# Kernel optimization log

Measured on AMD Instinct MI355X. Metric: run time of the kernel, lower is better.

## Reference

```python
import jax, jax.numpy as jnp
import numpy as np

B, S, D = 4, 2048, 1024
H = 16
HD = D // H

def setup_inputs() -> dict:
    key = jax.random.key(0)
    ks = jax.random.split(key, 6)
    std = 1.0 / np.sqrt(D)
    x = jax.random.normal(ks[0], (B, S, D), dtype=jnp.float32)
    Wq = jax.random.uniform(ks[1], (D, D), jnp.float32, -std, std)
    Wk = jax.random.uniform(ks[2], (D, D), jnp.float32, -std, std)
    Wv = jax.random.uniform(ks[3], (D, D), jnp.float32, -std, std)
    Wo = jax.random.uniform(ks[4], (D, D), jnp.float32, -std, std)
    bo = jax.random.uniform(ks[5], (D,), jnp.float32, -std, std)
    return {"x": x, "Wq": Wq, "Wk": Wk, "Wv": Wv, "Wo": Wo, "bo": bo}

def reference(x, Wq, Wk, Wv, Wo, bo):
    b, s, _ = x.shape
    # projections; torch Linear computes x @ W^T, here W stored as (d_in, d_out)... we use (D, D) applied as x @ W
    q = (x @ Wq).reshape(b, s, H, HD).transpose(0, 2, 1, 3)  # b h s hd
    k = (x @ Wk).reshape(b, s, H, HD).transpose(0, 2, 1, 3)
    v = (x @ Wv).reshape(b, s, H, HD).transpose(0, 2, 1, 3)
    scores = jnp.einsum('bhqd,bhkd->bhqk', q, k)
    causal = jnp.triu(jnp.ones((s, s), dtype=bool), k=1)
    scores = jnp.where(causal[None, None], -jnp.inf, scores)
    attn = jax.nn.softmax(scores / np.sqrt(HD), axis=-1)  # dropout=0.0 -> identity
    ctx = jnp.einsum('bhqk,bhkd->bhqd', attn, v)
    ctx = ctx.transpose(0, 2, 1, 3).reshape(b, s, D)
    return ctx @ Wo + bo
```

## Files before the change

kernel.cpp:

```cpp
#include <hip/hip_runtime.h>

typedef unsigned short u16;
typedef __bf16 bf16x8 __attribute__((ext_vector_type(8)));
typedef float f32x4 __attribute__((ext_vector_type(4)));

#define Bn 4
#define Sn 2048
#define Dn 1024
#define Hn 16
#define HDn 64

__device__ inline u16 f2bf(float f) {
  unsigned u = __builtin_bit_cast(unsigned, f);
  u += 0x7fffu + ((u >> 16) & 1u);
  return (u16)(u >> 16);
}

__device__ __forceinline__ void gl2lds16(const u16* g, u16* l) {
  __builtin_amdgcn_global_load_lds(
      (const __attribute__((address_space(1))) unsigned int*)g,
      (__attribute__((address_space(3))) unsigned int*)l, 16, 0, 0);
}

__device__ __forceinline__ float fexp2(float x) {
  return __builtin_amdgcn_exp2f(x);
}

__device__ __forceinline__ unsigned pk_bf_trunc(float lo, float hi) {
  return __builtin_amdgcn_perm(__builtin_bit_cast(unsigned, hi),
                               __builtin_bit_cast(unsigned, lo), 0x07060302u);
}

__global__ __launch_bounds__(256) void cvt4(const float* __restrict__ in,
                                            u16* __restrict__ out, int n4) {
  int i = blockIdx.x * 256 + threadIdx.x;
  if (i < n4) {
    float4 v = ((const float4*)in)[i];
    ushort4 o;
    o.x = f2bf(v.x); o.y = f2bf(v.y); o.z = f2bf(v.z); o.w = f2bf(v.w);
    ((ushort4*)out)[i] = o;
  }
}

__global__ __launch_bounds__(256) void tcvt(const float* __restrict__ in,
                                            u16* __restrict__ out, int n) {
  __shared__ u16 tile[32][33];
  int bx = blockIdx.x * 32;
  int by = blockIdx.y * 32;
  int tx = threadIdx.x & 31;
  int ty = threadIdx.x >> 5;
#pragma unroll
  for (int r = 0; r < 32; r += 8)
    tile[ty + r][tx] = f2bf(in[(size_t)(by + ty + r) * n + bx + tx]);
  __syncthreads();
#pragma unroll
  for (int r = 0; r < 32; r += 8)
    out[(size_t)(bx + ty + r) * n + by + tx] = tile[tx][ty + r];
}

__global__ __launch_bounds__(256) void gemm_qkv(const u16* __restrict__ A,
                                                const u16* __restrict__ Bt,
                                                u16* __restrict__ qkb,
                                                u16* __restrict__ vt,
                                                float qscale) {
  __shared__ __attribute__((aligned(16))) u16 As[128][32];
  __shared__ __attribute__((aligned(16))) u16 Bs[128][32];
  const int K = Dn;
  const int t = threadIdx.x;
  const int wave = t >> 6;
  const int lane = t & 63;
  const int lcol = lane & 15;
  const int quad = lane >> 4;
  const int wm = (wave >> 1) * 64;
  const int wn = (wave & 1) * 64;
  const int bm = blockIdx.y * 128;
  const int bn = blockIdx.x * 128;

  const int srow = lane >> 2;
  const int sseg = (lane & 3) * 8;
  const u16* a0p = A + (size_t)(bm + wave * 16 + srow) * K + sseg;
  const u16* a1p = a0p + (size_t)64 * K;
  const u16* b0p = Bt + (size_t)(bn + wave * 16 + srow) * K + sseg;
  const u16* b1p = b0p + (size_t)64 * K;
  u16* asl0 = &As[0][0] + wave * 512 + lane * 8;
  u16* asl1 = asl0 + 2048;
  u16* bsl0 = &Bs[0][0] + wave * 512 + lane * 8;
  u16* bsl1 = bsl0 + 2048;

  f32x4 acc[4][4];
#pragma unroll
  for (int i = 0; i < 4; i++)
#pragma unroll
    for (int j = 0; j < 4; j++) acc[i][j] = (f32x4){0.f, 0.f, 0.f, 0.f};

  for (int k0 = 0; k0 < K; k0 += 32) {
    gl2lds16(a0p + k0, asl0);
    gl2lds16(a1p + k0, asl1);
    gl2lds16(b0p + k0, bsl0);
    gl2lds16(b1p + k0, bsl1);
    __syncthreads();
    bf16x8 af[4], bf[4];
#pragma unroll
    for (int mi = 0; mi < 4; mi++)
      af[mi] = *(const bf16x8*)(&As[wm + mi * 16 + lcol][quad * 8]);
#pragma unroll
    for (int ni = 0; ni < 4; ni++)
      bf[ni] = *(const bf16x8*)(&Bs[wn + ni * 16 + lcol][quad * 8]);
#pragma unroll
    for (int mi = 0; mi < 4; mi++)
#pragma unroll
      for (int ni = 0; ni < 4; ni++)
        acc[mi][ni] = __builtin_amdgcn_mfma_f32_16x16x32_bf16(af[mi], bf[ni], acc[mi][ni], 0, 0, 0);
    __syncthreads();
  }

  if (bn >= 2048) {
    const int b = bm >> 11;
#pragma unroll
    for (int mi = 0; mi < 4; mi++) {
#pragma unroll
      for (int ni = 0; ni < 4; ni++) {
        int row0 = bm + wm + mi * 16 + quad * 4;
        int s = row0 & (Sn - 1);
        int vcol = bn + wn + ni * 16 + lcol - 2048;
        int bh = (b << 4) + (vcol >> 6);
        int hd = vcol & 63;
        unsigned d0 = (unsigned)f2bf(acc[mi][ni][0]) |
                      ((unsigned)f2bf(acc[mi][ni][1]) << 16);
        unsigned d1 = (unsigned)f2bf(acc[mi][ni][2]) |
                      ((unsigned)f2bf(acc[mi][ni][3]) << 16);
        *(uint2*)(vt + ((size_t)bh * HDn + hd) * Sn + s) = (uint2){d0, d1};
      }
    }
  } else {
    const float scale = (bn < 1024) ? qscale : 1.0f;
#pragma unroll
    for (int mi = 0; mi < 4; mi++) {
#pragma unroll
      for (int ni = 0; ni < 4; ni++) {
#pragma unroll
        for (int r = 0; r < 4; r++) {
          int row = bm + wm + mi * 16 + quad * 4 + r;
          int col = bn + wn + ni * 16 + lcol;
          qkb[(size_t)row * 2048 + col] = f2bf(acc[mi][ni][r] * scale);
        }
      }
    }
  }
}

__global__ __launch_bounds__(256) void gemm_out(const u16* __restrict__ A,
                                                const u16* __restrict__ Bt,
                                                float* __restrict__ Cout,
                                                const float* __restrict__ bias) {
  __shared__ __attribute__((aligned(16))) u16 As[128][32];
  __shared__ __attribute__((aligned(16))) u16 Bs[64][32];
  const int K = Dn;
  const int t = threadIdx.x;
  const int wave = t >> 6;
  const int lane = t & 63;
  const int lcol = lane & 15;
  const int quad = lane >> 4;
  const int wm = (wave >> 1) * 64;
  const int wn = (wave & 1) * 32;
  const int bm = blockIdx.y * 128;
  const int bn = blockIdx.x * 64;

  const int srow = lane >> 2;
  const int sseg = (lane & 3) * 8;
  const u16* a0p = A + (size_t)(bm + wave * 16 + srow) * K + sseg;
  const u16* a1p = a0p + (size_t)64 * K;
  const u16* b0p = Bt + (size_t)(bn + wave * 16 + srow) * K + sseg;
  u16* asl0 = &As[0][0] + wave * 512 + lane * 8;
  u16* asl1 = asl0 + 2048;
  u16* bsl0 = &Bs[0][0] + wave * 512 + lane * 8;

  f32x4 acc[4][2];
#pragma unroll
  for (int i = 0; i < 4; i++)
#pragma unroll
    for (int j = 0; j < 2; j++) acc[i][j] = (f32x4){0.f, 0.f, 0.f, 0.f};

  for (int k0 = 0; k0 < K; k0 += 32) {
    gl2lds16(a0p + k0, asl0);
    gl2lds16(a1p + k0, asl1);
    gl2lds16(b0p + k0, bsl0);
    __syncthreads();
    bf16x8 af[4], bf[2];
#pragma unroll
    for (int mi = 0; mi < 4; mi++)
      af[mi] = *(const bf16x8*)(&As[wm + mi * 16 + lcol][quad * 8]);
#pragma unroll
    for (int ni = 0; ni < 2; ni++)
      bf[ni] = *(const bf16x8*)(&Bs[wn + ni * 16 + lcol][quad * 8]);
#pragma unroll
    for (int mi = 0; mi < 4; mi++)
#pragma unroll
      for (int ni = 0; ni < 2; ni++)
        acc[mi][ni] = __builtin_amdgcn_mfma_f32_16x16x32_bf16(af[mi], bf[ni], acc[mi][ni], 0, 0, 0);
    __syncthreads();
  }

#pragma unroll
  for (int mi = 0; mi < 4; mi++) {
#pragma unroll
    for (int ni = 0; ni < 2; ni++) {
#pragma unroll
      for (int r = 0; r < 4; r++) {
        int row = bm + wm + mi * 16 + quad * 4 + r;
        int col = bn + wn + ni * 16 + lcol;
        Cout[(size_t)row * Dn + col] = acc[mi][ni][r] + bias[col];
      }
    }
  }
}

__global__ __launch_bounds__(256, 4) void attn4(const u16* __restrict__ QK,
                                                const u16* __restrict__ Vt,
                                                u16* __restrict__ ctx) {
  __shared__ __attribute__((aligned(16))) u16 Ks2[2][64][32];
  __shared__ __attribute__((aligned(16))) u16 Vts2[2][64][32];
  __shared__ __attribute__((aligned(16))) u16 Pt[4][32][72];

  const int bh = blockIdx.x;
  const int b = bh >> 4, h = bh & 15;
  const int q0 = (15 - blockIdx.y) * 128;
  const int t = threadIdx.x;
  const int w = t >> 6;
  const int lane = t & 63;
  const int lcol = lane & 15;
  const int quad = lane >> 4;
  const int qw = q0 + w * 32;

  const size_t qkbase = ((size_t)b * Sn) * 2048 + h * HDn;
  const size_t obase = ((size_t)b * Sn) * Dn + h * HDn;
  const size_t vbase = ((size_t)bh * HDn) * Sn;

  bf16x8 qf[2][2];
#pragma unroll
  for (int qb = 0; qb < 2; qb++) {
    const u16* qp = QK + qkbase + (size_t)(qw + qb * 16 + lcol) * 2048 + quad * 8;
    qf[qb][0] = *(const bf16x8*)qp;
    qf[qb][1] = *(const bf16x8*)(qp + 32);
  }

  f32x4 o[2][4];
#pragma unroll
  for (int qb = 0; qb < 2; qb++)
#pragma unroll
    for (int nb = 0; nb < 4; nb++) o[qb][nb] = (f32x4){0.f, 0.f, 0.f, 0.f};
  float lsum[2] = {0.f, 0.f};

  const int srow = lane >> 2;
  const int sseg = (lane & 3) * 8;
  const u16* kp0 = QK + qkbase + 1024 + (size_t)(w * 16 + srow) * 2048 + sseg;
  const u16* vp0 = Vt + vbase + (size_t)(w * 16 + srow) * Sn + sseg;
  u16* ksl0 = &Ks2[0][0][0] + w * 512 + lane * 8;
  u16* ksl1 = ksl0 + 2048;
  u16* vsl0 = &Vts2[0][0][0] + w * 512 + lane * 8;
  u16* vsl1 = vsl0 + 2048;

  const int n_kv = q0 + 128;

  for (int j0 = 0; j0 < n_kv; j0 += 64) {
    {
      const u16* kp = kp0 + (size_t)j0 * 2048;
      gl2lds16(kp, ksl0);
      gl2lds16(kp + 32, ksl1);
      const u16* vp = vp0 + j0;
      gl2lds16(vp, vsl0);
      gl2lds16(vp + 32, vsl1);
    }
    __syncthreads();

    if (j0 <= qw + 31) {
      f32x4 s[4][2];
#pragma unroll
      for (int mb = 0; mb < 4; mb++) {
        bf16x8 kf0 = *(const bf16x8*)(&Ks2[0][mb * 16 + lcol][quad * 8]);
        bf16x8 kf1 = *(const bf16x8*)(&Ks2[1][mb * 16 + lcol][quad * 8]);
#pragma unroll
        for (int qb = 0; qb < 2; qb++) {
          f32x4 a = (f32x4){0.f, 0.f, 0.f, 0.f};
          a = __builtin_amdgcn_mfma_f32_16x16x32_bf16(kf0, qf[qb][0], a, 0, 0, 0);
          a = __builtin_amdgcn_mfma_f32_16x16x32_bf16(kf1, qf[qb][1], a, 0, 0, 0);
          s[mb][qb] = a;
        }
      }

      const bool needmask = (j0 + 63 > qw);
#pragma unroll
      for (int qb = 0; qb < 2; qb++) {
        const int qrow = qw + qb * 16 + lcol;
#pragma unroll
        for (int mb = 0; mb < 4; mb++) {
          float p[4];
#pragma unroll
          for (int r = 0; r < 4; r++) p[r] = fexp2(s[mb][qb][r]);
          if (needmask) {
            const int kvb = j0 + mb * 16 + quad * 4;
#pragma unroll
            for (int r = 0; r < 4; r++)
              if (kvb + r > qrow) p[r] = 0.f;
          }
          lsum[qb] += (p[0] + p[1]) + (p[2] + p[3]);
          unsigned d0 = pk_bf_trunc(p[0], p[1]);
          unsigned d1 = pk_bf_trunc(p[2], p[3]);
          *(uint2*)(&Pt[w][qb * 16 + lcol][mb * 16 + quad * 4]) = (uint2){d0, d1};
        }
      }

#pragma unroll
      for (int c = 0; c < 2; c++) {
        bf16x8 pf0 = *(const bf16x8*)(&Pt[w][lcol][c * 32 + quad * 8]);
        bf16x8 pf1 = *(const bf16x8*)(&Pt[w][16 + lcol][c * 32 + quad * 8]);
#pragma unroll
        for (int nb = 0; nb < 4; nb++) {
          bf16x8 vf = *(const bf16x8*)(&Vts2[c][nb * 16 + lcol][quad * 8]);
          o[0][nb] = __builtin_amdgcn_mfma_f32_16x16x32_bf16(vf, pf0, o[0][nb], 0, 0, 0);
          o[1][nb] = __builtin_amdgcn_mfma_f32_16x16x32_bf16(vf, pf1, o[1][nb], 0, 0, 0);
        }
      }
    }
    __syncthreads();
  }

#pragma unroll
  for (int qb = 0; qb < 2; qb++) {
    float l = lsum[qb];
    l += __shfl_xor(l, 16);
    l += __shfl_xor(l, 32);
    float inv = 1.0f / l;
#pragma unroll
    for (int nb = 0; nb < 4; nb++) {
      unsigned d0 = (unsigned)f2bf(o[qb][nb][0] * inv) |
                    ((unsigned)f2bf(o[qb][nb][1] * inv) << 16);
      unsigned d1 = (unsigned)f2bf(o[qb][nb][2] * inv) |
                    ((unsigned)f2bf(o[qb][nb][3] * inv) << 16);
      u16* p = ctx + obase + (size_t)(qw + qb * 16 + lcol) * Dn + nb * 16 + quad * 4;
      *(uint2*)p = (uint2){d0, d1};
    }
  }
}

extern "C" void kernel_launch(void* const* d_in, const int* in_sizes, int n_in,
                              void* d_out, int out_size, void* d_ws, size_t ws_size,
                              hipStream_t stream) {
  const float* x  = (const float*)d_in[0];
  const float* Wq = (const float*)d_in[1];
  const float* Wk = (const float*)d_in[2];
  const float* Wv = (const float*)d_in[3];
  const float* Wo = (const float*)d_in[4];
  const float* bo = (const float*)d_in[5];
  float* out = (float*)d_out;

  const size_t BSD = (size_t)Bn * Sn * Dn;
  const size_t DD = (size_t)Dn * Dn;

  u16* xb    = (u16*)d_ws;
  u16* wqkvt = xb + BSD;
  u16* wot   = wqkvt + 3 * DD;
  u16* qkb   = wot + DD;
  u16* vt    = qkb + 2 * BSD;
  u16* cb    = vt + BSD;

  cvt4<<<(int)(BSD / 4 / 256), 256, 0, stream>>>(x, xb, (int)(BSD / 4));
  dim3 tg(Dn / 32, Dn / 32);
  tcvt<<<tg, 256, 0, stream>>>(Wq, wqkvt, Dn);
  tcvt<<<tg, 256, 0, stream>>>(Wk, wqkvt + DD, Dn);
  tcvt<<<tg, 256, 0, stream>>>(Wv, wqkvt + 2 * DD, Dn);
  tcvt<<<tg, 256, 0, stream>>>(Wo, wot, Dn);

  gemm_qkv<<<dim3(3072 / 128, (Bn * Sn) / 128), 256, 0, stream>>>(
      xb, wqkvt, qkb, vt, 0.125f * 1.44269504f);

  attn4<<<dim3(Bn * Hn, 16), 256, 0, stream>>>(qkb, vt, cb);

  gemm_out<<<dim3(Dn / 64, (Bn * Sn) / 128), 256, 0, stream>>>(cb, wot, out, bo);
}
```

Measured before the change: 263.8 us.

## Pair causal query tiles in attention, deepen GEMM K-step, merge weight conversions

The attention kernel now gives each block two query tiles, one near the start and one near the end of the sequence, so every block does balanced causal work, and it halves the grid to 8 blocks per head. The K/V tile loaded into shared memory is reused by both strips. Both GEMMs now load 64 K-elements per barrier pair instead of 32, halving synchronisations at the cost of doubled LDS. The four weight transpose-converts are merged into one launch with a z-dimension. Risks are higher register pressure in attention (launch bounds lowered to 2) and fewer blocks in flight.

Result: faster. 246.7 us (-6.5%).

```diff
diff --git a/kernel.cpp b/kernel.cpp
--- a/kernel.cpp
+++ b/kernel.cpp
@@ -42,20 +42,26 @@
   }
 }
 
-__global__ __launch_bounds__(256) void tcvt(const float* __restrict__ in,
-                                            u16* __restrict__ out, int n) {
+__global__ __launch_bounds__(256) void tcvt4(const float* __restrict__ w0,
+                                             const float* __restrict__ w1,
+                                             const float* __restrict__ w2,
+                                             const float* __restrict__ w3,
+                                             u16* __restrict__ out) {
   __shared__ u16 tile[32][33];
+  const float* in = (blockIdx.z == 0) ? w0 : (blockIdx.z == 1) ? w1
+                   : (blockIdx.z == 2) ? w2 : w3;
+  u16* dst = out + (size_t)blockIdx.z * Dn * Dn;
   int bx = blockIdx.x * 32;
   int by = blockIdx.y * 32;
   int tx = threadIdx.x & 31;
   int ty = threadIdx.x >> 5;
 #pragma unroll
   for (int r = 0; r < 32; r += 8)
-    tile[ty + r][tx] = f2bf(in[(size_t)(by + ty + r) * n + bx + tx]);
+    tile[ty + r][tx] = f2bf(in[(size_t)(by + ty + r) * Dn + bx + tx]);
   __syncthreads();
 #pragma unroll
   for (int r = 0; r < 32; r += 8)
-    out[(size_t)(bx + ty + r) * n + by + tx] = tile[tx][ty + r];
+    dst[(size_t)(bx + ty + r) * Dn + by + tx] = tile[tx][ty + r];
 }
 
 __global__ __launch_bounds__(256) void gemm_qkv(const u16* __restrict__ A,
@@ -63,8 +69,8 @@
                                                 u16* __restrict__ qkb,
                                                 u16* __restrict__ vt,
                                                 float qscale) {
-  __shared__ __attribute__((aligned(16))) u16 As[128][32];
-  __shared__ __attribute__((aligned(16))) u16 Bs[128][32];
+  __shared__ __attribute__((aligned(16))) u16 As[2][128][32];
+  __shared__ __attribute__((aligned(16))) u16 Bs[2][128][32];
   const int K = Dn;
   const int t = threadIdx.x;
   const int wave = t >> 6;
@@ -82,9 +88,9 @@
   const u16* a1p = a0p + (size_t)64 * K;
   const u16* b0p = Bt + (size_t)(bn + wave * 16 + srow) * K + sseg;
   const u16* b1p = b0p + (size_t)64 * K;
-  u16* asl0 = &As[0][0] + wave * 512 + lane * 8;
+  u16* asl0 = &As[0][0][0] + wave * 512 + lane * 8;
   u16* asl1 = asl0 + 2048;
-  u16* bsl0 = &Bs[0][0] + wave * 512 + lane * 8;
+  u16* bsl0 = &Bs[0][0][0] + wave * 512 + lane * 8;
   u16* bsl1 = bsl0 + 2048;
 
   f32x4 acc[4][4];
@@ -93,24 +99,31 @@
 #pragma unroll
     for (int j = 0; j < 4; j++) acc[i][j] = (f32x4){0.f, 0.f, 0.f, 0.f};
 
-  for (int k0 = 0; k0 < K; k0 += 32) {
+  for (int k0 = 0; k0 < K; k0 += 64) {
     gl2lds16(a0p + k0, asl0);
     gl2lds16(a1p + k0, asl1);
+    gl2lds16(a0p + k0 + 32, asl0 + 4096);
+    gl2lds16(a1p + k0 + 32, asl1 + 4096);
     gl2lds16(b0p + k0, bsl0);
     gl2lds16(b1p + k0, bsl1);
-    __syncthreads();
-    bf16x8 af[4], bf[4];
-#pragma unroll
-    for (int mi = 0; mi < 4; mi++)
-      af[mi] = *(const bf16x8*)(&As[wm + mi * 16 + lcol][quad * 8]);
-#pragma unroll
-    for (int ni = 0; ni < 4; ni++)
-      bf[ni] = *(const bf16x8*)(&Bs[wn + ni * 16 + lcol][quad * 8]);
-#pragma unroll
-    for (int mi = 0; mi < 4; mi++)
+    gl2lds16(b0p + k0 + 32, bsl0 + 4096);
+    gl2lds16(b1p + k0 + 32, bsl1 + 4096);
+    __syncthreads();
+#pragma unroll
+    for (int ks = 0; ks < 2; ks++) {
+      bf16x8 af[4], bf[4];
+#pragma unroll
+      for (int mi = 0; mi < 4; mi++)
+        af[mi] = *(const bf16x8*)(&As[ks][wm + mi * 16 + lcol][quad * 8]);
 #pragma unroll
       for (int ni = 0; ni < 4; ni++)
-        acc[mi][ni] = __builtin_amdgcn_mfma_f32_16x16x32_bf16(af[mi], bf[ni], acc[mi][ni], 0, 0, 0);
+        bf[ni] = *(const bf16x8*)(&Bs[ks][wn + ni * 16 + lcol][quad * 8]);
+#pragma unroll
+      for (int mi = 0; mi < 4; mi++)
+#pragma unroll
+        for (int ni = 0; ni < 4; ni++)
+          acc[mi][ni] = __builtin_amdgcn_mfma_f32_16x16x32_bf16(af[mi], bf[ni], acc[mi][ni], 0, 0, 0);
+    }
     __syncthreads();
   }
 
@@ -153,8 +166,8 @@
                                                 const u16* __restrict__ Bt,
                                                 float* __restrict__ Cout,
                                                 const float* __restrict__ bias) {
-  __shared__ __attribute__((aligned(16))) u16 As[128][32];
-  __shared__ __attribute__((aligned(16))) u16 Bs[64][32];
+  __shared__ __attribute__((aligned(16))) u16 As[2][128][32];
+  __shared__ __attribute__((aligned(16))) u16 Bs[2][64][32];
   const int K = Dn;
   const int t = threadIdx.x;
   const int wave = t >> 6;
@@ -171,9 +184,9 @@
   const u16* a0p = A + (size_t)(bm + wave * 16 + srow) * K + sseg;
   const u16* a1p = a0p + (size_t)64 * K;
   const u16* b0p = Bt + (size_t)(bn + wave * 16 + srow) * K + sseg;
-  u16* asl0 = &As[0][0] + wave * 512 + lane * 8;
+  u16* asl0 = &As[0][0][0] + wave * 512 + lane * 8;
   u16* asl1 = asl0 + 2048;
-  u16* bsl0 = &Bs[0][0] + wave * 512 + lane * 8;
+  u16* bsl0 = &Bs[0][0][0] + wave * 512 + lane * 8;
 
   f32x4 acc[4][2];
 #pragma unroll
@@ -181,23 +194,29 @@
 #pragma unroll
     for (int j = 0; j < 2; j++) acc[i][j] = (f32x4){0.f, 0.f, 0.f, 0.f};
 
-  for (int k0 = 0; k0 < K; k0 += 32) {
+  for (int k0 = 0; k0 < K; k0 += 64) {
     gl2lds16(a0p + k0, asl0);
     gl2lds16(a1p + k0, asl1);
+    gl2lds16(a0p + k0 + 32, asl0 + 4096);
+    gl2lds16(a1p + k0 + 32, asl1 + 4096);
     gl2lds16(b0p + k0, bsl0);
-    __syncthreads();
-    bf16x8 af[4], bf[2];
-#pragma unroll
-    for (int mi = 0; mi < 4; mi++)
-      af[mi] = *(const bf16x8*)(&As[wm + mi * 16 + lcol][quad * 8]);
-#pragma unroll
-    for (int ni = 0; ni < 2; ni++)
-      bf[ni] = *(const bf16x8*)(&Bs[wn + ni * 16 + lcol][quad * 8]);
-#pragma unroll
-    for (int mi = 0; mi < 4; mi++)
+    gl2lds16(b0p + k0 + 32, bsl0 + 2048);
+    __syncthreads();
+#pragma unroll
+    for (int ks = 0; ks < 2; ks++) {
+      bf16x8 af[4], bf[2];
+#pragma unroll
+      for (int mi = 0; mi < 4; mi++)
+        af[mi] = *(const bf16x8*)(&As[ks][wm + mi * 16 + lcol][quad * 8]);
 #pragma unroll
       for (int ni = 0; ni < 2; ni++)
-        acc[mi][ni] = __builtin_amdgcn_mfma_f32_16x16x32_bf16(af[mi], bf[ni], acc[mi][ni], 0, 0, 0);
+        bf[ni] = *(const bf16x8*)(&Bs[ks][wn + ni * 16 + lcol][quad * 8]);
+#pragma unroll
+      for (int mi = 0; mi < 4; mi++)
+#pragma unroll
+        for (int ni = 0; ni < 2; ni++)
+          acc[mi][ni] = __builtin_amdgcn_mfma_f32_16x16x32_bf16(af[mi], bf[ni], acc[mi][ni], 0, 0, 0);
+    }
     __syncthreads();
   }
 
@@ -215,7 +234,7 @@
   }
 }
 
-__global__ __launch_bounds__(256, 4) void attn4(const u16* __restrict__ QK,
+__global__ __launch_bounds__(256, 2) void attn5(const u16* __restrict__ QK,
                                                 const u16* __restrict__ Vt,
                                                 u16* __restrict__ ctx) {
   __shared__ __attribute__((aligned(16))) u16 Ks2[2][64][32];
@@ -224,32 +243,39 @@
 
   const int bh = blockIdx.x;
   const int b = bh >> 4, h = bh & 15;
-  const int q0 = (15 - blockIdx.y) * 128;
+  const int pair = blockIdx.y;
   const int t = threadIdx.x;
   const int w = t >> 6;
   const int lane = t & 63;
   const int lcol = lane & 15;
   const int quad = lane >> 4;
-  const int qw = q0 + w * 32;
+  const int qw0 = pair * 128 + w * 32;
+  const int qw1 = (15 - pair) * 128 + w * 32;
 
   const size_t qkbase = ((size_t)b * Sn) * 2048 + h * HDn;
   const size_t obase = ((size_t)b * Sn) * Dn + h * HDn;
   const size_t vbase = ((size_t)bh * HDn) * Sn;
 
-  bf16x8 qf[2][2];
-#pragma unroll
-  for (int qb = 0; qb < 2; qb++) {
-    const u16* qp = QK + qkbase + (size_t)(qw + qb * 16 + lcol) * 2048 + quad * 8;
-    qf[qb][0] = *(const bf16x8*)qp;
-    qf[qb][1] = *(const bf16x8*)(qp + 32);
-  }
-
-  f32x4 o[2][4];
-#pragma unroll
-  for (int qb = 0; qb < 2; qb++)
-#pragma unroll
-    for (int nb = 0; nb < 4; nb++) o[qb][nb] = (f32x4){0.f, 0.f, 0.f, 0.f};
-  float lsum[2] = {0.f, 0.f};
+  bf16x8 qf[2][2][2];
+#pragma unroll
+  for (int si = 0; si < 2; si++) {
+    const int qws = si ? qw1 : qw0;
+#pragma unroll
+    for (int qb = 0; qb < 2; qb++) {
+      const u16* qp = QK + qkbase + (size_t)(qws + qb * 16 + lcol) * 2048 + quad * 8;
+      qf[si][qb][0] = *(const bf16x8*)qp;
+      qf[si][qb][1] = *(const bf16x8*)(qp + 32);
+    }
+  }
+
+  f32x4 o[2][2][4];
+#pragma unroll
+  for (int si = 0; si < 2; si++)
+#pragma unroll
+    for (int qb = 0; qb < 2; qb++)
+#pragma unroll
+      for (int nb = 0; nb < 4; nb++) o[si][qb][nb] = (f32x4){0.f, 0.f, 0.f, 0.f};
+  float lsum[2][2] = {{0.f, 0.f}, {0.f, 0.f}};
 
   const int srow = lane >> 2;
   const int sseg = (lane & 3) * 8;
@@ -260,7 +286,57 @@
   u16* vsl0 = &Vts2[0][0][0] + w * 512 + lane * 8;
   u16* vsl1 = vsl0 + 2048;
 
-  const int n_kv = q0 + 128;
+  auto do_strip = [&](int si, int qw, int j0) {
+    f32x4 s[4][2];
+#pragma unroll
+    for (int mb = 0; mb < 4; mb++) {
+      bf16x8 kf0 = *(const bf16x8*)(&Ks2[0][mb * 16 + lcol][quad * 8]);
+      bf16x8 kf1 = *(const bf16x8*)(&Ks2[1][mb * 16 + lcol][quad * 8]);
+#pragma unroll
+      for (int qb = 0; qb < 2; qb++) {
+        f32x4 a = (f32x4){0.f, 0.f, 0.f, 0.f};
+        a = __builtin_amdgcn_mfma_f32_16x16x32_bf16(kf0, qf[si][qb][0], a, 0, 0, 0);
+        a = __builtin_amdgcn_mfma_f32_16x16x32_bf16(kf1, qf[si][qb][1], a, 0, 0, 0);
+        s[mb][qb] = a;
+      }
+    }
+
+    const bool needmask = (j0 + 63 > qw);
+#pragma unroll
+    for (int qb = 0; qb < 2; qb++) {
+      const int qrow = qw + qb * 16 + lcol;
+#pragma unroll
+      for (int mb = 0; mb < 4; mb++) {
+        float p[4];
+#pragma unroll
+        for (int r = 0; r < 4; r++) p[r] = fexp2(s[mb][qb][r]);
+        if (needmask) {
+          const int kvb = j0 + mb * 16 + quad * 4;
+#pragma unroll
+          for (int r = 0; r < 4; r++)
+            if (kvb + r > qrow) p[r] = 0.f;
+        }
+        lsum[si][qb] += (p[0] + p[1]) + (p[2] + p[3]);
+        unsigned d0 = pk_bf_trunc(p[0], p[1]);
+        unsigned d1 = pk_bf_trunc(p[2], p[3]);
+        *(uint2*)(&Pt[w][qb * 16 + lcol][mb * 16 + quad * 4]) = (uint2){d0, d1};
+      }
+    }
+
+#pragma unroll
+    for (int c = 0; c < 2; c++) {
+      bf16x8 pf0 = *(const bf16x8*)(&Pt[w][lcol][c * 32 + quad * 8]);
+      bf16x8 pf1 = *(const bf16x8*)(&Pt[w][16 + lcol][c * 32 + quad * 8]);
+#pragma unroll
+      for (int nb = 0; nb < 4; nb++) {
+        bf16x8 vf = *(const bf16x8*)(&Vts2[c][nb * 16 + lcol][quad * 8]);
+        o[si][0][nb] = __builtin_amdgcn_mfma_f32_16x16x32_bf16(vf, pf0, o[si][0][nb], 0, 0, 0);
+        o[si][1][nb] = __builtin_amdgcn_mfma_f32_16x16x32_bf16(vf, pf1, o[si][1][nb], 0, 0, 0);
+      }
+    }
+  };
+
+  const int n_kv = (15 - pair) * 128 + 128;
 
   for (int j0 = 0; j0 < n_kv; j0 += 64) {
     {
@@ -273,72 +349,29 @@
     }
     __syncthreads();
 
-    if (j0 <= qw + 31) {
-      f32x4 s[4][2];
-#pragma unroll
-      for (int mb = 0; mb < 4; mb++) {
-        bf16x8 kf0 = *(const bf16x8*)(&Ks2[0][mb * 16 + lcol][quad * 8]);
-        bf16x8 kf1 = *(const bf16x8*)(&Ks2[1][mb * 16 + lcol][quad * 8]);
-#pragma unroll
-        for (int qb = 0; qb < 2; qb++) {
-          f32x4 a = (f32x4){0.f, 0.f, 0.f, 0.f};
-          a = __builtin_amdgcn_mfma_f32_16x16x32_bf16(kf0, qf[qb][0], a, 0, 0, 0);
-          a = __builtin_amdgcn_mfma_f32_16x16x32_bf16(kf1, qf[qb][1], a, 0, 0, 0);
-          s[mb][qb] = a;
-        }
-      }
-
-      const bool needmask = (j0 + 63 > qw);
-#pragma unroll
-      for (int qb = 0; qb < 2; qb++) {
-        const int qrow = qw + qb * 16 + lcol;
-#pragma unroll
-        for (int mb = 0; mb < 4; mb++) {
-          float p[4];
-#pragma unroll
-          for (int r = 0; r < 4; r++) p[r] = fexp2(s[mb][qb][r]);
-          if (needmask) {
-            const int kvb = j0 + mb * 16 + quad * 4;
-#pragma unroll
-            for (int r = 0; r < 4; r++)
-              if (kvb + r > qrow) p[r] = 0.f;
-          }
-          lsum[qb] += (p[0] + p[1]) + (p[2] + p[3]);
-          unsigned d0 = pk_bf_trunc(p[0], p[1]);
-          unsigned d1 = pk_bf_trunc(p[2], p[3]);
-          *(uint2*)(&Pt[w][qb * 16 + lcol][mb * 16 + quad * 4]) = (uint2){d0, d1};
-        }
-      }
-
-#pragma unroll
-      for (int c = 0; c < 2; c++) {
-        bf16x8 pf0 = *(const bf16x8*)(&Pt[w][lcol][c * 32 + quad * 8]);
-        bf16x8 pf1 = *(const bf16x8*)(&Pt[w][16 + lcol][c * 32 + quad * 8]);
-#pragma unroll
-        for (int nb = 0; nb < 4; nb++) {
-          bf16x8 vf = *(const bf16x8*)(&Vts2[c][nb * 16 + lcol][quad * 8]);
-          o[0][nb] = __builtin_amdgcn_mfma_f32_16x16x32_bf16(vf, pf0, o[0][nb], 0, 0, 0);
-          o[1][nb] = __builtin_amdgcn_mfma_f32_16x16x32_bf16(vf, pf1, o[1][nb], 0, 0, 0);
-        }
-      }
-    }
-    __syncthreads();
-  }
-
-#pragma unroll
-  for (int qb = 0; qb < 2; qb++) {
-    float l = lsum[qb];
-    l += __shfl_xor(l, 16);
-    l += __shfl_xor(l, 32);
-    float inv = 1.0f / l;
-#pragma unroll
-    for (int nb = 0; nb < 4; nb++) {
-      unsigned d0 = (unsigned)f2bf(o[qb][nb][0] * inv) |
-                    ((unsigned)f2bf(o[qb][nb][1] * inv) << 16);
-      unsigned d1 = (unsigned)f2bf(o[qb][nb][2] * inv) |
-                    ((unsigned)f2bf(o[qb][nb][3] * inv) << 16);
-      u16* p = ctx + obase + (size_t)(qw + qb * 16 + lcol) * Dn + nb * 16 + quad * 4;
-      *(uint2*)p = (uint2){d0, d1};
+    if (j0 <= qw1 + 31) do_strip(1, qw1, j0);
+    if (j0 <= qw0 + 31) do_strip(0, qw0, j0);
+    __syncthreads();
+  }
+
+#pragma unroll
+  for (int si = 0; si < 2; si++) {
+    const int qws = si ? qw1 : qw0;
+#pragma unroll
+    for (int qb = 0; qb < 2; qb++) {
+      float l = lsum[si][qb];
+      l += __shfl_xor(l, 16);
+      l += __shfl_xor(l, 32);
+      float inv = 1.0f / l;
+#pragma unroll
+      for (int nb = 0; nb < 4; nb++) {
+        unsigned d0 = (unsigned)f2bf(o[si][qb][nb][0] * inv) |
+                      ((unsigned)f2bf(o[si][qb][nb][1] * inv) << 16);
+        unsigned d1 = (unsigned)f2bf(o[si][qb][nb][2] * inv) |
+                      ((unsigned)f2bf(o[si][qb][nb][3] * inv) << 16);
+        u16* p = ctx + obase + (size_t)(qws + qb * 16 + lcol) * Dn + nb * 16 + quad * 4;
+        *(uint2*)p = (uint2){d0, d1};
+      }
     }
   }
 }
@@ -358,23 +391,18 @@
   const size_t DD = (size_t)Dn * Dn;
 
   u16* xb    = (u16*)d_ws;
-  u16* wqkvt = xb + BSD;
-  u16* wot   = wqkvt + 3 * DD;
-  u16* qkb   = wot + DD;
+  u16* wall  = xb + BSD;
+  u16* qkb   = wall + 4 * DD;
   u16* vt    = qkb + 2 * BSD;
   u16* cb    = vt + BSD;
 
   cvt4<<<(int)(BSD / 4 / 256), 256, 0, stream>>>(x, xb, (int)(BSD / 4));
-  dim3 tg(Dn / 32, Dn / 32);
-  tcvt<<<tg, 256, 0, stream>>>(Wq, wqkvt, Dn);
-  tcvt<<<tg, 256, 0, stream>>>(Wk, wqkvt + DD, Dn);
-  tcvt<<<tg, 256, 0, stream>>>(Wv, wqkvt + 2 * DD, Dn);
-  tcvt<<<tg, 256, 0, stream>>>(Wo, wot, Dn);
+  tcvt4<<<dim3(Dn / 32, Dn / 32, 4), 256, 0, stream>>>(Wq, Wk, Wv, Wo, wall);
 
   gemm_qkv<<<dim3(3072 / 128, (Bn * Sn) / 128), 256, 0, stream>>>(
-      xb, wqkvt, qkb, vt, 0.125f * 1.44269504f);
-
-  attn4<<<dim3(Bn * Hn, 16), 256, 0, stream>>>(qkb, vt, cb);
-
-  gemm_out<<<dim3(Dn / 64, (Bn * Sn) / 128), 256, 0, stream>>>(cb, wot, out, bo);
-}
+      xb, wall, qkb, vt, 0.125f * 1.44269504f);
+
+  attn5<<<dim3(Bn * Hn, 8), 256, 0, stream>>>(qkb, vt, cb);
+
+  gemm_out<<<dim3(Dn / 64, (Bn * Sn) / 128), 256, 0, stream>>>(cb, wall + 3 * DD, out, bo);
+}
```
